# Performance work log

Measured on AMD Instinct MI355X. Metric: run time of the kernel, lower is better.

## Reference

```python
import jax, jax.numpy as jnp
import numpy as np

N = 131072      # batch of states
Q = 8           # q_ndim (dof_ndim)
DZ = 2 * Q      # state dim [q, p]
H = 256         # hidden_size
ALPHA_RATIO = 100000.0 / (100000.0 + 100000.0)  # 0.5


def setup_inputs() -> dict:
    key = jax.random.key(0)
    ks = jax.random.split(key, 12)
    def w(i, shape, scale=0.05):
        return jax.random.normal(ks[i], shape, dtype=jnp.float32) * scale
    return {
        "t": jnp.zeros((), jnp.float32),
        "z": jax.random.normal(ks[0], (N, DZ), jnp.float32),
        # h_net hidden layers (the output Linear of h_net only feeds a print, omitted)
        "hW1": w(1, (H, DZ)), "hb1": w(2, (H,)),
        "hW2": w(3, (H, H)), "hb2": w(4, (H,)),
        # flex_net layers
        "fW1": w(5, (H, DZ)), "fb1": w(6, (H,)),
        "fW2": w(7, (H, H)), "fb2": w(8, (H,)),
        "fW3": w(9, (DZ, H)), "fb3": w(10, (DZ,)),
    }


def reference(t, z, hW1, hb1, hW2, hb2, fW1, fb1, fW2, fb2, fW3, fb3):
    ar = ALPHA_RATIO
    # h_net hidden pass; sps[i] = d tanh(a)/da = 1 - tanh(a)^2 (autograd.grad in torch)
    a1 = z @ hW1.T + hb1            # (N, H)
    t1 = jnp.tanh(a1)
    s1 = 1.0 - t1 * t1              # sps[0]
    a2 = t1 @ hW2.T + hb2           # (N, H)
    t2 = jnp.tanh(a2)
    s2 = 1.0 - t2 * t2              # sps[1]
    # flex_net pass, mixing flex activations with h-net tanh derivatives (reversed order)
    f = z @ fW1.T + fb1
    f = (1.0 - ar) * f * s2 + ar * jnp.tanh(f)   # idx = 1 -> sps[1]
    f = f @ fW2.T + fb2
    f = (1.0 - ar) * f * s1 + ar * jnp.tanh(f)   # idx = 0 -> sps[0]
    f = f @ fW3.T + fb3             # (N, DZ)
    # angular_dims is empty -> CosSin is identity -> its batched jacobian D is
    # the identity matrix per sample, so bmm(f[:,None,:], D) == f.
    out = f
    # symplectic J: dz/dt = [dH/dp, -dH/dq]
    dz_dt = jnp.concatenate([out[:, Q:], -out[:, :Q]], axis=-1)
    return dz_dt
```

## Files before the change

### kernel.cpp

```cpp
#include <hip/hip_runtime.h>
#include <hip/hip_bf16.h>
#include <stdint.h>


typedef __attribute__((ext_vector_type(8))) short short8;
typedef __attribute__((ext_vector_type(4))) float floatx4;

static __device__ __forceinline__ unsigned short f2bf(float x) {
  union { float f; uint32_t u; } v; v.f = x;
  return (unsigned short)((v.u + 0x7FFFu + ((v.u >> 16) & 1u)) >> 16);
}
static __device__ __forceinline__ float bf2f(uint32_t bits16) {
  union { uint32_t u; float f; } v; v.u = bits16 << 16;
  return v.f;
}
static __device__ __forceinline__ float unpk(uint32_t p, int hi) {
  return bf2f(hi ? (p >> 16) : (p & 0xffffu));
}
static __device__ __forceinline__ float tanh_fast(float x) {
  float cx = fminf(4.0f, fmaxf(-4.0f, x));
  float x2 = cx * cx;
  float num = cx * (135135.0f + x2 * (17325.0f + x2 * (378.0f + x2)));
  float den = 135135.0f + x2 * (62370.0f + x2 * (3150.0f + 28.0f * x2));
  return num * __builtin_amdgcn_rcpf(den);
}

__global__ __launch_bounds__(256) void prep_kernel(
    const float* __restrict__ hW1, const float* __restrict__ hW2,
    const float* __restrict__ fW1, const float* __restrict__ fW2,
    const float* __restrict__ fW3, unsigned short* __restrict__ ws) {
  int i = blockIdx.x * 256 + threadIdx.x;
  ws[16384 + i] = f2bf(hW2[i]);
  ws[81920 + i] = f2bf(fW2[i]);
  if (i < 8192) {
    int r = i >> 5, c = i & 31;
    unsigned short vh = 0, vf = 0;
    if (c < 16) { vh = f2bf(hW1[r * 16 + c]); vf = f2bf(fW1[r * 16 + c]); }
    ws[i] = vh;
    ws[8192 + i] = vf;
  }
  if (i < 4096) ws[147456 + i] = f2bf(fW3[i]);
}

__global__ __launch_bounds__(256, 2) void flexhnn_kernel(
    const float* __restrict__ z,
    const float* __restrict__ hb1, const float* __restrict__ hb2,
    const float* __restrict__ fb1, const float* __restrict__ fb2,
    const float* __restrict__ fb3,
    const unsigned short* __restrict__ ws,
    float* __restrict__ out) {
  __shared__ __align__(16) unsigned short z_bf[64 * 32];
  __shared__ __align__(16) unsigned short act[64 * 264];

  const int tid = threadIdx.x;
  const int lane = tid & 63;
  const int wave = tid >> 6;
  const int laneCol = lane & 15;
  const int kg = lane >> 4;
  const int wc = wave * 64;
  const int row0 = blockIdx.x * 64;

  const unsigned short* w1h = ws;
  const unsigned short* w1f = ws + 8192;
  const unsigned short* w2h = ws + 16384;
  const unsigned short* w2f = ws + 81920;
  const unsigned short* w3f = ws + 147456;

  {
    int r = tid >> 2;
    int c = (tid & 3) * 4;
    float4 zv = *reinterpret_cast<const float4*>(z + (size_t)(row0 + r) * 16 + c);
    unsigned short* p = &z_bf[r * 32 + c];
    p[0] = f2bf(zv.x); p[1] = f2bf(zv.y); p[2] = f2bf(zv.z); p[3] = f2bf(zv.w);
    unsigned short* q = &z_bf[r * 32 + 16 + c];
    q[0] = 0; q[1] = 0; q[2] = 0; q[3] = 0;
  }
  __syncthreads();

  float hb1v[4], hb2v[4], fb1v[4], fb2v[4];
#pragma unroll
  for (int nf = 0; nf < 4; ++nf) {
    int col = wc + nf * 16 + laneCol;
    hb1v[nf] = hb1[col]; hb2v[nf] = hb2[col];
    fb1v[nf] = fb1[col]; fb2v[nf] = fb2[col];
  }

  uint32_t s1p[4][4][2];

  {
    short8 az[4];
#pragma unroll
    for (int mf = 0; mf < 4; ++mf)
      az[mf] = *reinterpret_cast<const short8*>(&z_bf[(mf * 16 + laneCol) * 32 + kg * 8]);
#pragma unroll
    for (int nf = 0; nf < 4; ++nf) {
      int col = wc + nf * 16 + laneCol;
      short8 b = *reinterpret_cast<const short8*>(&w1h[col * 32 + kg * 8]);
#pragma unroll
      for (int mf = 0; mf < 4; ++mf) {
        floatx4 c0 = {0.f, 0.f, 0.f, 0.f};
        floatx4 a1 = __builtin_amdgcn_mfma_f32_16x16x32_bf16(az[mf], b, c0, 0, 0, 0);
        unsigned short tb[4], sb[4];
#pragma unroll
        for (int r = 0; r < 4; ++r) {
          float t = tanh_fast(a1[r] + hb1v[nf]);
          tb[r] = f2bf(t);
          sb[r] = f2bf(1.0f - t * t);
        }
        s1p[mf][nf][0] = (uint32_t)sb[0] | ((uint32_t)sb[1] << 16);
        s1p[mf][nf][1] = (uint32_t)sb[2] | ((uint32_t)sb[3] << 16);
#pragma unroll
        for (int r = 0; r < 4; ++r)
          act[(mf * 16 + kg * 4 + r) * 264 + col] = tb[r];
      }
    }
  }
  __syncthreads();

  uint32_t s2p[4][4][2];
  {
    floatx4 acc[4][4];
#pragma unroll
    for (int mf = 0; mf < 4; ++mf)
#pragma unroll
      for (int nf = 0; nf < 4; ++nf)
        acc[mf][nf] = (floatx4){0.f, 0.f, 0.f, 0.f};
#pragma unroll 2
    for (int ks = 0; ks < 8; ++ks) {
      int k0 = ks * 32;
      short8 a[4], b[4];
#pragma unroll
      for (int mf = 0; mf < 4; ++mf)
        a[mf] = *reinterpret_cast<const short8*>(&act[(mf * 16 + laneCol) * 264 + k0 + kg * 8]);
#pragma unroll
      for (int nf = 0; nf < 4; ++nf)
        b[nf] = *reinterpret_cast<const short8*>(&w2h[(wc + nf * 16 + laneCol) * 256 + k0 + kg * 8]);
#pragma unroll
      for (int mf = 0; mf < 4; ++mf)
#pragma unroll
        for (int nf = 0; nf < 4; ++nf)
          acc[mf][nf] = __builtin_amdgcn_mfma_f32_16x16x32_bf16(a[mf], b[nf], acc[mf][nf], 0, 0, 0);
    }
#pragma unroll
    for (int mf = 0; mf < 4; ++mf)
#pragma unroll
      for (int nf = 0; nf < 4; ++nf) {
        unsigned short sb[4];
#pragma unroll
        for (int r = 0; r < 4; ++r) {
          float t = tanh_fast(acc[mf][nf][r] + hb2v[nf]);
          sb[r] = f2bf(1.0f - t * t);
        }
        s2p[mf][nf][0] = (uint32_t)sb[0] | ((uint32_t)sb[1] << 16);
        s2p[mf][nf][1] = (uint32_t)sb[2] | ((uint32_t)sb[3] << 16);
      }
  }

  floatx4 accf[4][4];
  {
    short8 az[4];
#pragma unroll
    for (int mf = 0; mf < 4; ++mf)
      az[mf] = *reinterpret_cast<const short8*>(&z_bf[(mf * 16 + laneCol) * 32 + kg * 8]);
#pragma unroll
    for (int nf = 0; nf < 4; ++nf) {
      short8 b = *reinterpret_cast<const short8*>(&w1f[(wc + nf * 16 + laneCol) * 32 + kg * 8]);
#pragma unroll
      for (int mf = 0; mf < 4; ++mf) {
        floatx4 c0 = {0.f, 0.f, 0.f, 0.f};
        accf[mf][nf] = __builtin_amdgcn_mfma_f32_16x16x32_bf16(az[mf], b, c0, 0, 0, 0);
      }
    }
  }
  __syncthreads();

#pragma unroll
  for (int mf = 0; mf < 4; ++mf)
#pragma unroll
    for (int nf = 0; nf < 4; ++nf) {
      int col = wc + nf * 16 + laneCol;
#pragma unroll
      for (int r = 0; r < 4; ++r) {
        float fv = accf[mf][nf][r] + fb1v[nf];
        float s2 = unpk(s2p[mf][nf][r >> 1], r & 1);
        float fm = 0.5f * (fv * s2 + tanh_fast(fv));
        act[(mf * 16 + kg * 4 + r) * 264 + col] = f2bf(fm);
      }
    }
  __syncthreads();

  {
    floatx4 acc[4][4];
#pragma unroll
    for (int mf = 0; mf < 4; ++mf)
#pragma unroll
      for (int nf = 0; nf < 4; ++nf)
        acc[mf][nf] = (floatx4){0.f, 0.f, 0.f, 0.f};
#pragma unroll 2
    for (int ks = 0; ks < 8; ++ks) {
      int k0 = ks * 32;
      short8 a[4], b[4];
#pragma unroll
      for (int mf = 0; mf < 4; ++mf)
        a[mf] = *reinterpret_cast<const short8*>(&act[(mf * 16 + laneCol) * 264 + k0 + kg * 8]);
#pragma unroll
      for (int nf = 0; nf < 4; ++nf)
        b[nf] = *reinterpret_cast<const short8*>(&w2f[(wc + nf * 16 + laneCol) * 256 + k0 + kg * 8]);
#pragma unroll
      for (int mf = 0; mf < 4; ++mf)
#pragma unroll
        for (int nf = 0; nf < 4; ++nf)
          acc[mf][nf] = __builtin_amdgcn_mfma_f32_16x16x32_bf16(a[mf], b[nf], acc[mf][nf], 0, 0, 0);
    }
    __syncthreads();
#pragma unroll
    for (int mf = 0; mf < 4; ++mf)
#pragma unroll
      for (int nf = 0; nf < 4; ++nf) {
        int col = wc + nf * 16 + laneCol;
#pragma unroll
        for (int r = 0; r < 4; ++r) {
          float fv = acc[mf][nf][r] + fb2v[nf];
          float s1 = unpk(s1p[mf][nf][r >> 1], r & 1);
          float fm = 0.5f * (fv * s1 + tanh_fast(fv));
          act[(mf * 16 + kg * 4 + r) * 264 + col] = f2bf(fm);
        }
      }
  }
  __syncthreads();

  {
    floatx4 a4 = {0.f, 0.f, 0.f, 0.f};
#pragma unroll 2
    for (int ks = 0; ks < 8; ++ks) {
      int k0 = ks * 32;
      short8 a = *reinterpret_cast<const short8*>(&act[(wave * 16 + laneCol) * 264 + k0 + kg * 8]);
      short8 b = *reinterpret_cast<const short8*>(&w3f[laneCol * 256 + k0 + kg * 8]);
      a4 = __builtin_amdgcn_mfma_f32_16x16x32_bf16(a, b, a4, 0, 0, 0);
    }
    int o = laneCol;
    float bb3 = fb3[o];
    int oc = (o < 8) ? (o + 8) : (o - 8);
    float sgn = (o < 8) ? -1.0f : 1.0f;
#pragma unroll
    for (int r = 0; r < 4; ++r) {
      int grow = row0 + wave * 16 + kg * 4 + r;
      out[(size_t)grow * 16 + oc] = sgn * (a4[r] + bb3);
    }
  }
}

extern "C" void kernel_launch(void* const* d_in, const int* in_sizes, int n_in,
                              void* d_out, int out_size, void* d_ws, size_t ws_size,
                              hipStream_t stream) {
  const float* z   = (const float*)d_in[1];
  const float* hW1 = (const float*)d_in[2];
  const float* hb1 = (const float*)d_in[3];
  const float* hW2 = (const float*)d_in[4];
  const float* hb2 = (const float*)d_in[5];
  const float* fW1 = (const float*)d_in[6];
  const float* fb1 = (const float*)d_in[7];
  const float* fW2 = (const float*)d_in[8];
  const float* fb2 = (const float*)d_in[9];
  const float* fW3 = (const float*)d_in[10];
  const float* fb3 = (const float*)d_in[11];
  unsigned short* ws = (unsigned short*)d_ws;
  float* out = (float*)d_out;

  hipLaunchKernelGGL(prep_kernel, dim3(256), dim3(256), 0, stream,
                     hW1, hW2, fW1, fW2, fW3, ws);
  hipLaunchKernelGGL(flexhnn_kernel, dim3(131072 / 64), dim3(256), 0, stream,
                     z, hb1, hb2, fb1, fb2, fb3, (const unsigned short*)ws, out);
}
```

Before: 184.4 us.

## Compute transposed MLP per wave with register-resident activations and fragment-packed weights

Restructures the fused MLP so each wave independently handles 32 batch rows in transposed form (weights as the A operand, activations as the B operand). Activations stay in registers between layers, because the MFMA output layout directly feeds the next layer's B fragment, which removes the LDS activation staging and all block-wide barriers. The prep kernel now pre-permutes the weights into MFMA fragment order so each lane loads its fragment with one contiguous 16-byte read, and biases are folded into the accumulator init. The trade-offs are much higher register pressure, since three sets of 2x8 uintx4 activation arrays are live, and every wave now re-reads the full weight matrices from global/L2 instead of sharing them across the block.

Measured after the change: 225.7 us. 22.4% more time.

```diff
diff --git a/kernel.cpp b/kernel.cpp
--- a/kernel.cpp
+++ b/kernel.cpp
@@ -5,17 +5,22 @@
 
 typedef __attribute__((ext_vector_type(8))) short short8;
 typedef __attribute__((ext_vector_type(4))) float floatx4;
+typedef __attribute__((ext_vector_type(4))) unsigned int uintx4;
 
 static __device__ __forceinline__ unsigned short f2bf(float x) {
   union { float f; uint32_t u; } v; v.f = x;
   return (unsigned short)((v.u + 0x7FFFu + ((v.u >> 16) & 1u)) >> 16);
 }
-static __device__ __forceinline__ float bf2f(uint32_t bits16) {
-  union { uint32_t u; float f; } v; v.u = bits16 << 16;
+static __device__ __forceinline__ uint32_t packpair(float a, float b) {
+  return (uint32_t)f2bf(a) | ((uint32_t)f2bf(b) << 16);
+}
+static __device__ __forceinline__ float unpklo(uint32_t u) {
+  union { uint32_t u; float f; } v; v.u = u << 16;
   return v.f;
 }
-static __device__ __forceinline__ float unpk(uint32_t p, int hi) {
-  return bf2f(hi ? (p >> 16) : (p & 0xffffu));
+static __device__ __forceinline__ float unpkhi(uint32_t u) {
+  union { uint32_t u; float f; } v; v.u = u & 0xffff0000u;
+  return v.f;
 }
 static __device__ __forceinline__ float tanh_fast(float x) {
   float cx = fminf(4.0f, fmaxf(-4.0f, x));
@@ -24,22 +29,40 @@
   float den = 135135.0f + x2 * (62370.0f + x2 * (3150.0f + 28.0f * x2));
   return num * __builtin_amdgcn_rcpf(den);
 }
+static __device__ __forceinline__ floatx4 mfma16(short8 a, short8 b, floatx4 c) {
+  return __builtin_amdgcn_mfma_f32_16x16x32_bf16(a, b, c, 0, 0, 0);
+}
+static __device__ __forceinline__ short8 asfrag(uintx4 u) {
+  union { uintx4 u; short8 s; } v; v.u = u;
+  return v.s;
+}
 
 __global__ __launch_bounds__(256) void prep_kernel(
     const float* __restrict__ hW1, const float* __restrict__ hW2,
     const float* __restrict__ fW1, const float* __restrict__ fW2,
     const float* __restrict__ fW3, unsigned short* __restrict__ ws) {
   int i = blockIdx.x * 256 + threadIdx.x;
-  ws[16384 + i] = f2bf(hW2[i]);
-  ws[81920 + i] = f2bf(fW2[i]);
+  {
+    int ob = i >> 12, s = (i >> 9) & 7, lane = (i >> 3) & 63, j = i & 7;
+    int m = ob * 16 + (lane & 15), kg = lane >> 4;
+    int k = 32 * s + 16 * (j >> 2) + 4 * kg + (j & 3);
+    ws[16384 + i] = f2bf(hW2[m * 256 + k]);
+    ws[81920 + i] = f2bf(fW2[m * 256 + k]);
+  }
   if (i < 8192) {
-    int r = i >> 5, c = i & 31;
+    int ob = i >> 9, lane = (i >> 3) & 63, j = i & 7;
+    int m = ob * 16 + (lane & 15), kg = lane >> 4;
     unsigned short vh = 0, vf = 0;
-    if (c < 16) { vh = f2bf(hW1[r * 16 + c]); vf = f2bf(fW1[r * 16 + c]); }
+    if (kg < 2) { int k = kg * 8 + j; vh = f2bf(hW1[m * 16 + k]); vf = f2bf(fW1[m * 16 + k]); }
     ws[i] = vh;
     ws[8192 + i] = vf;
   }
-  if (i < 4096) ws[147456 + i] = f2bf(fW3[i]);
+  if (i < 4096) {
+    int s = i >> 9, lane = (i >> 3) & 63, j = i & 7;
+    int m = lane & 15, kg = lane >> 4;
+    int k = 32 * s + 16 * (j >> 2) + 4 * kg + (j & 3);
+    ws[147456 + i] = f2bf(fW3[m * 256 + k]);
+  }
 }
 
 __global__ __launch_bounds__(256, 2) void flexhnn_kernel(
@@ -49,203 +72,121 @@
     const float* __restrict__ fb3,
     const unsigned short* __restrict__ ws,
     float* __restrict__ out) {
-  __shared__ __align__(16) unsigned short z_bf[64 * 32];
-  __shared__ __align__(16) unsigned short act[64 * 264];
-
-  const int tid = threadIdx.x;
-  const int lane = tid & 63;
-  const int wave = tid >> 6;
-  const int laneCol = lane & 15;
-  const int kg = lane >> 4;
-  const int wc = wave * 64;
-  const int row0 = blockIdx.x * 64;
-
-  const unsigned short* w1h = ws;
-  const unsigned short* w1f = ws + 8192;
-  const unsigned short* w2h = ws + 16384;
-  const unsigned short* w2f = ws + 81920;
-  const unsigned short* w3f = ws + 147456;
+  __shared__ uint32_t s1_lds[4][2][32][64];
+
+  const int tid = threadIdx.x, lane = tid & 63, wave = tid >> 6;
+  const int c = lane & 15, kg = lane >> 4;
+  const int b0 = (blockIdx.x * 4 + wave) * 32;
+
+  const unsigned short* w1hp = ws;
+  const unsigned short* w1fp = ws + 8192;
+  const unsigned short* w2hp = ws + 16384;
+  const unsigned short* w2fp = ws + 81920;
+  const unsigned short* w3fp = ws + 147456;
+
+  short8 zf[2];
+  zf[0] = (short8){0,0,0,0,0,0,0,0};
+  zf[1] = (short8){0,0,0,0,0,0,0,0};
+  if (kg < 2) {
+#pragma unroll
+    for (int st = 0; st < 2; ++st) {
+      const float* zr = z + (size_t)(b0 + st * 16 + c) * 16 + kg * 8;
+      uintx4 u;
+      u.x = packpair(zr[0], zr[1]); u.y = packpair(zr[2], zr[3]);
+      u.z = packpair(zr[4], zr[5]); u.w = packpair(zr[6], zr[7]);
+      zf[st] = asfrag(u);
+    }
+  }
+
+  uintx4 t1v[2][8];
+#pragma unroll
+  for (int ob = 0; ob < 16; ++ob) {
+    short8 wf = *reinterpret_cast<const short8*>(w1hp + (ob * 64 + lane) * 8);
+    floatx4 bias = *reinterpret_cast<const floatx4*>(hb1 + ob * 16 + kg * 4);
+#pragma unroll
+    for (int st = 0; st < 2; ++st) {
+      floatx4 a = mfma16(wf, zf[st], bias);
+      float t0 = tanh_fast(a[0]), t1_ = tanh_fast(a[1]);
+      float t2 = tanh_fast(a[2]), t3 = tanh_fast(a[3]);
+      t1v[st][ob >> 1][(ob & 1) * 2 + 0] = packpair(t0, t1_);
+      t1v[st][ob >> 1][(ob & 1) * 2 + 1] = packpair(t2, t3);
+      s1_lds[wave][st][ob * 2 + 0][lane] = packpair(1.0f - t0 * t0, 1.0f - t1_ * t1_);
+      s1_lds[wave][st][ob * 2 + 1][lane] = packpair(1.0f - t2 * t2, 1.0f - t3 * t3);
+    }
+  }
+
+  uintx4 fmv[2][8];
+#pragma unroll
+  for (int ob = 0; ob < 16; ++ob) {
+    floatx4 b2 = *reinterpret_cast<const floatx4*>(hb2 + ob * 16 + kg * 4);
+    floatx4 a[2] = {b2, b2};
+#pragma unroll
+    for (int s = 0; s < 8; ++s) {
+      short8 wf = *reinterpret_cast<const short8*>(w2hp + ((ob * 8 + s) * 64 + lane) * 8);
+      a[0] = mfma16(wf, asfrag(t1v[0][s]), a[0]);
+      a[1] = mfma16(wf, asfrag(t1v[1][s]), a[1]);
+    }
+    short8 w1 = *reinterpret_cast<const short8*>(w1fp + (ob * 64 + lane) * 8);
+    floatx4 bf1 = *reinterpret_cast<const floatx4*>(fb1 + ob * 16 + kg * 4);
+#pragma unroll
+    for (int st = 0; st < 2; ++st) {
+      floatx4 f = mfma16(w1, zf[st], bf1);
+      float fm[4];
+#pragma unroll
+      for (int r = 0; r < 4; ++r) {
+        float t2 = tanh_fast(a[st][r]);
+        float s2 = 1.0f - t2 * t2;
+        float fv = f[r];
+        fm[r] = 0.5f * (fv * s2 + tanh_fast(fv));
+      }
+      fmv[st][ob >> 1][(ob & 1) * 2 + 0] = packpair(fm[0], fm[1]);
+      fmv[st][ob >> 1][(ob & 1) * 2 + 1] = packpair(fm[2], fm[3]);
+    }
+  }
+
+  uintx4 gv[2][8];
+#pragma unroll
+  for (int ob = 0; ob < 16; ++ob) {
+    floatx4 bf2 = *reinterpret_cast<const floatx4*>(fb2 + ob * 16 + kg * 4);
+    floatx4 a[2] = {bf2, bf2};
+#pragma unroll
+    for (int s = 0; s < 8; ++s) {
+      short8 wf = *reinterpret_cast<const short8*>(w2fp + ((ob * 8 + s) * 64 + lane) * 8);
+      a[0] = mfma16(wf, asfrag(fmv[0][s]), a[0]);
+      a[1] = mfma16(wf, asfrag(fmv[1][s]), a[1]);
+    }
+#pragma unroll
+    for (int st = 0; st < 2; ++st) {
+      uint32_t sp0 = s1_lds[wave][st][ob * 2 + 0][lane];
+      uint32_t sp1 = s1_lds[wave][st][ob * 2 + 1][lane];
+      float s1a = unpklo(sp0), s1b = unpkhi(sp0), s1c = unpklo(sp1), s1d = unpkhi(sp1);
+      float f0 = a[st][0], f1_ = a[st][1], f2_ = a[st][2], f3 = a[st][3];
+      float g0 = 0.5f * (f0 * s1a + tanh_fast(f0));
+      float g1 = 0.5f * (f1_ * s1b + tanh_fast(f1_));
+      float g2 = 0.5f * (f2_ * s1c + tanh_fast(f2_));
+      float g3 = 0.5f * (f3 * s1d + tanh_fast(f3));
+      gv[st][ob >> 1][(ob & 1) * 2 + 0] = packpair(g0, g1);
+      gv[st][ob >> 1][(ob & 1) * 2 + 1] = packpair(g2, g3);
+    }
+  }
 
   {
-    int r = tid >> 2;
-    int c = (tid & 3) * 4;
-    float4 zv = *reinterpret_cast<const float4*>(z + (size_t)(row0 + r) * 16 + c);
-    unsigned short* p = &z_bf[r * 32 + c];
-    p[0] = f2bf(zv.x); p[1] = f2bf(zv.y); p[2] = f2bf(zv.z); p[3] = f2bf(zv.w);
-    unsigned short* q = &z_bf[r * 32 + 16 + c];
-    q[0] = 0; q[1] = 0; q[2] = 0; q[3] = 0;
-  }
-  __syncthreads();
-
-  float hb1v[4], hb2v[4], fb1v[4], fb2v[4];
-#pragma unroll
-  for (int nf = 0; nf < 4; ++nf) {
-    int col = wc + nf * 16 + laneCol;
-    hb1v[nf] = hb1[col]; hb2v[nf] = hb2[col];
-    fb1v[nf] = fb1[col]; fb2v[nf] = fb2[col];
-  }
-
-  uint32_t s1p[4][4][2];
-
-  {
-    short8 az[4];
-#pragma unroll
-    for (int mf = 0; mf < 4; ++mf)
-      az[mf] = *reinterpret_cast<const short8*>(&z_bf[(mf * 16 + laneCol) * 32 + kg * 8]);
-#pragma unroll
-    for (int nf = 0; nf < 4; ++nf) {
-      int col = wc + nf * 16 + laneCol;
-      short8 b = *reinterpret_cast<const short8*>(&w1h[col * 32 + kg * 8]);
-#pragma unroll
-      for (int mf = 0; mf < 4; ++mf) {
-        floatx4 c0 = {0.f, 0.f, 0.f, 0.f};
-        floatx4 a1 = __builtin_amdgcn_mfma_f32_16x16x32_bf16(az[mf], b, c0, 0, 0, 0);
-        unsigned short tb[4], sb[4];
-#pragma unroll
-        for (int r = 0; r < 4; ++r) {
-          float t = tanh_fast(a1[r] + hb1v[nf]);
-          tb[r] = f2bf(t);
-          sb[r] = f2bf(1.0f - t * t);
-        }
-        s1p[mf][nf][0] = (uint32_t)sb[0] | ((uint32_t)sb[1] << 16);
-        s1p[mf][nf][1] = (uint32_t)sb[2] | ((uint32_t)sb[3] << 16);
-#pragma unroll
-        for (int r = 0; r < 4; ++r)
-          act[(mf * 16 + kg * 4 + r) * 264 + col] = tb[r];
-      }
-    }
-  }
-  __syncthreads();
-
-  uint32_t s2p[4][4][2];
-  {
-    floatx4 acc[4][4];
-#pragma unroll
-    for (int mf = 0; mf < 4; ++mf)
-#pragma unroll
-      for (int nf = 0; nf < 4; ++nf)
-        acc[mf][nf] = (floatx4){0.f, 0.f, 0.f, 0.f};
-#pragma unroll 2
-    for (int ks = 0; ks < 8; ++ks) {
-      int k0 = ks * 32;
-      short8 a[4], b[4];
-#pragma unroll
-      for (int mf = 0; mf < 4; ++mf)
-        a[mf] = *reinterpret_cast<const short8*>(&act[(mf * 16 + laneCol) * 264 + k0 + kg * 8]);
-#pragma unroll
-      for (int nf = 0; nf < 4; ++nf)
-        b[nf] = *reinterpret_cast<const short8*>(&w2h[(wc + nf * 16 + laneCol) * 256 + k0 + kg * 8]);
-#pragma unroll
-      for (int mf = 0; mf < 4; ++mf)
-#pragma unroll
-        for (int nf = 0; nf < 4; ++nf)
-          acc[mf][nf] = __builtin_amdgcn_mfma_f32_16x16x32_bf16(a[mf], b[nf], acc[mf][nf], 0, 0, 0);
-    }
-#pragma unroll
-    for (int mf = 0; mf < 4; ++mf)
-#pragma unroll
-      for (int nf = 0; nf < 4; ++nf) {
-        unsigned short sb[4];
-#pragma unroll
-        for (int r = 0; r < 4; ++r) {
-          float t = tanh_fast(acc[mf][nf][r] + hb2v[nf]);
-          sb[r] = f2bf(1.0f - t * t);
-        }
-        s2p[mf][nf][0] = (uint32_t)sb[0] | ((uint32_t)sb[1] << 16);
-        s2p[mf][nf][1] = (uint32_t)sb[2] | ((uint32_t)sb[3] << 16);
-      }
-  }
-
-  floatx4 accf[4][4];
-  {
-    short8 az[4];
-#pragma unroll
-    for (int mf = 0; mf < 4; ++mf)
-      az[mf] = *reinterpret_cast<const short8*>(&z_bf[(mf * 16 + laneCol) * 32 + kg * 8]);
-#pragma unroll
-    for (int nf = 0; nf < 4; ++nf) {
-      short8 b = *reinterpret_cast<const short8*>(&w1f[(wc + nf * 16 + laneCol) * 32 + kg * 8]);
-#pragma unroll
-      for (int mf = 0; mf < 4; ++mf) {
-        floatx4 c0 = {0.f, 0.f, 0.f, 0.f};
-        accf[mf][nf] = __builtin_amdgcn_mfma_f32_16x16x32_bf16(az[mf], b, c0, 0, 0, 0);
-      }
-    }
-  }
-  __syncthreads();
-
-#pragma unroll
-  for (int mf = 0; mf < 4; ++mf)
-#pragma unroll
-    for (int nf = 0; nf < 4; ++nf) {
-      int col = wc + nf * 16 + laneCol;
-#pragma unroll
-      for (int r = 0; r < 4; ++r) {
-        float fv = accf[mf][nf][r] + fb1v[nf];
-        float s2 = unpk(s2p[mf][nf][r >> 1], r & 1);
-        float fm = 0.5f * (fv * s2 + tanh_fast(fv));
-        act[(mf * 16 + kg * 4 + r) * 264 + col] = f2bf(fm);
-      }
-    }
-  __syncthreads();
-
-  {
-    floatx4 acc[4][4];
-#pragma unroll
-    for (int mf = 0; mf < 4; ++mf)
-#pragma unroll
-      for (int nf = 0; nf < 4; ++nf)
-        acc[mf][nf] = (floatx4){0.f, 0.f, 0.f, 0.f};
-#pragma unroll 2
-    for (int ks = 0; ks < 8; ++ks) {
-      int k0 = ks * 32;
-      short8 a[4], b[4];
-#pragma unroll
-      for (int mf = 0; mf < 4; ++mf)
-        a[mf] = *reinterpret_cast<const short8*>(&act[(mf * 16 + laneCol) * 264 + k0 + kg * 8]);
-#pragma unroll
-      for (int nf = 0; nf < 4; ++nf)
-        b[nf] = *reinterpret_cast<const short8*>(&w2f[(wc + nf * 16 + laneCol) * 256 + k0 + kg * 8]);
-#pragma unroll
-      for (int mf = 0; mf < 4; ++mf)
-#pragma unroll
-        for (int nf = 0; nf < 4; ++nf)
-          acc[mf][nf] = __builtin_amdgcn_mfma_f32_16x16x32_bf16(a[mf], b[nf], acc[mf][nf], 0, 0, 0);
-    }
-    __syncthreads();
-#pragma unroll
-    for (int mf = 0; mf < 4; ++mf)
-#pragma unroll
-      for (int nf = 0; nf < 4; ++nf) {
-        int col = wc + nf * 16 + laneCol;
-#pragma unroll
-        for (int r = 0; r < 4; ++r) {
-          float fv = acc[mf][nf][r] + fb2v[nf];
-          float s1 = unpk(s1p[mf][nf][r >> 1], r & 1);
-          float fm = 0.5f * (fv * s1 + tanh_fast(fv));
-          act[(mf * 16 + kg * 4 + r) * 264 + col] = f2bf(fm);
-        }
-      }
-  }
-  __syncthreads();
-
-  {
-    floatx4 a4 = {0.f, 0.f, 0.f, 0.f};
-#pragma unroll 2
-    for (int ks = 0; ks < 8; ++ks) {
-      int k0 = ks * 32;
-      short8 a = *reinterpret_cast<const short8*>(&act[(wave * 16 + laneCol) * 264 + k0 + kg * 8]);
-      short8 b = *reinterpret_cast<const short8*>(&w3f[laneCol * 256 + k0 + kg * 8]);
-      a4 = __builtin_amdgcn_mfma_f32_16x16x32_bf16(a, b, a4, 0, 0, 0);
-    }
-    int o = laneCol;
-    float bb3 = fb3[o];
-    int oc = (o < 8) ? (o + 8) : (o - 8);
-    float sgn = (o < 8) ? -1.0f : 1.0f;
-#pragma unroll
-    for (int r = 0; r < 4; ++r) {
-      int grow = row0 + wave * 16 + kg * 4 + r;
-      out[(size_t)grow * 16 + oc] = sgn * (a4[r] + bb3);
+    floatx4 b3 = *reinterpret_cast<const floatx4*>(fb3 + kg * 4);
+    floatx4 o[2] = {b3, b3};
+#pragma unroll
+    for (int s = 0; s < 8; ++s) {
+      short8 wf = *reinterpret_cast<const short8*>(w3fp + (s * 64 + lane) * 8);
+      o[0] = mfma16(wf, asfrag(gv[0][s]), o[0]);
+      o[1] = mfma16(wf, asfrag(gv[1][s]), o[1]);
+    }
+    const int off = (kg < 2) ? (kg * 4 + 8) : (kg * 4 - 8);
+    const float sgn = (kg < 2) ? -1.0f : 1.0f;
+#pragma unroll
+    for (int st = 0; st < 2; ++st) {
+      float4 stv;
+      stv.x = sgn * o[st][0]; stv.y = sgn * o[st][1];
+      stv.z = sgn * o[st][2]; stv.w = sgn * o[st][3];
+      *reinterpret_cast<float4*>(out + (size_t)(b0 + st * 16 + c) * 16 + off) = stv;
     }
   }
 }
@@ -269,6 +210,6 @@
 
   hipLaunchKernelGGL(prep_kernel, dim3(256), dim3(256), 0, stream,
                      hW1, hW2, fW1, fW2, fW3, ws);
-  hipLaunchKernelGGL(flexhnn_kernel, dim3(131072 / 64), dim3(256), 0, stream,
+  hipLaunchKernelGGL(flexhnn_kernel, dim3(1024), dim3(256), 0, stream,
                      z, hb1, hb2, fb1, fb2, fb3, (const unsigned short*)ws, out);
 }
```
